# Performance work log

Measured on AMD Instinct MI355X. Metric: run time of the kernel, lower is better.

Reference implementation:

```python
import jax, jax.numpy as jnp
import numpy as np

EPS = 1e-5
B, CIN, L = 512, 5, 1024   # batch, input channels, msp length == d_model
COUT, A, NB = 32, 13, 5    # CNN branch channels, max_atoms, num_bonds_prediction


def conv1d(x, w, pad, groups=1):
    # x: (N, C, L), w: (O, I/groups, K)
    return jax.lax.conv_general_dilated(
        x, w, window_strides=(1,), padding=[(pad, pad)],
        dimension_numbers=("NCH", "OIH", "NCH"), feature_group_count=groups)


def batchnorm(x, g, b):
    # training-mode BN over (N, L) per channel, as nn.BatchNorm1d in train()
    m = jnp.mean(x, axis=(0, 2), keepdims=True)
    v = jnp.var(x, axis=(0, 2), keepdims=True)
    return (x - m) * jax.lax.rsqrt(v + EPS) * g[None, :, None] + b[None, :, None]


def setup_inputs() -> dict:
    key = jax.random.key(0)
    ks = jax.random.split(key, 16)
    n = jax.random.normal
    inp = {
        "src": n(ks[0], (B, CIN, L), dtype=jnp.float32),
        "mask": jnp.ones((B, A), dtype=bool),
        "max_atoms": A,
        # CNN branch 1 (kernel 5) : depthwise, pointwise, BN, residual 1x1 conv
        "dw1": n(ks[1], (CIN, 1, 5), dtype=jnp.float32) * 0.2,
        "pw1": n(ks[2], (COUT, CIN, 1), dtype=jnp.float32) * 0.2,
        "g1": jnp.ones((COUT,), jnp.float32),
        "be1": jnp.zeros((COUT,), jnp.float32),
        "r1w": n(ks[3], (COUT, CIN, 1), dtype=jnp.float32) * 0.2,
        "r1b": jnp.zeros((COUT,), jnp.float32),
        # CNN branch 2 (kernel 3)
        "dw2": n(ks[4], (CIN, 1, 3), dtype=jnp.float32) * 0.2,
        "pw2": n(ks[5], (COUT, CIN, 1), dtype=jnp.float32) * 0.2,
        "g2": jnp.ones((COUT,), jnp.float32),
        "be2": jnp.zeros((COUT,), jnp.float32),
        "r2w": n(ks[6], (COUT, CIN, 1), dtype=jnp.float32) * 0.2,
        "r2b": jnp.zeros((COUT,), jnp.float32),
        # EdgeClassify2 linears: ll1 (2*COUT -> A), fl (2*L -> NB)
        "ll1w": n(ks[7], (A, 2 * COUT), dtype=jnp.float32) * 0.1,
        "ll1b": jnp.zeros((A,), jnp.float32),
        "flw": n(ks[8], (NB, 2 * L), dtype=jnp.float32) * 0.02,
        "flb": jnp.zeros((NB,), jnp.float32),
    }
    return inp


def reference(src, mask, max_atoms, dw1, pw1, g1, be1, r1w, r1b,
              dw2, pw2, g2, be2, r2w, r2b, ll1w, ll1b, flw, flb):
    # ---- CNN encoder ----
    e1 = jax.nn.relu(batchnorm(conv1d(conv1d(src, dw1, 2, groups=CIN), pw1, 0), g1, be1))
    e1 = e1 * (conv1d(src, r1w, 0) + r1b[None, :, None])
    e2 = jax.nn.relu(batchnorm(conv1d(conv1d(src, dw2, 1, groups=CIN), pw2, 0), g2, be2))
    e2 = e2 * (conv1d(src, r2w, 0) + r2b[None, :, None])
    x = jnp.concatenate([e1, e2], axis=1)          # (B, 2*COUT, L)
    # ---- EdgeClassify2 ----
    # ll1 over channel dim: (B, 2*COUT, L) -> (B, A, L)
    h = jnp.einsum("bcl,ac->bal", x, ll1w) + ll1b[None, :, None]
    # vectorized replacement of the O(A^2) python loop:
    # final_e[:, i, j] = concat(h[:, min(i,j)], h[:, max(i,j)])
    idx = jnp.arange(max_atoms)
    mn = jnp.minimum(idx[:, None], idx[None, :])   # (A, A)
    mx = jnp.maximum(idx[:, None], idx[None, :])
    final_e = jnp.concatenate([h[:, mn, :], h[:, mx, :]], axis=-1)  # (B, A, A, 2L)
    out = jnp.einsum("bijd,nd->bijn", final_e, flw) + flb           # (B, A, A, NB)
    return out
```

## Files before the change

kernel.cpp:

```cpp
#include <hip/hip_runtime.h>
#include <hip/hip_bf16.h>

#define BB 512
#define LL 1024
#define AA 13
#define NBP 5
#define NTOT (BB * LL)
#define EPSV 1e-5f

#define WS_F     192
#define WS_PART  256
#define WS_CONST 10496
#define WS_FLW   16384

typedef __attribute__((ext_vector_type(8))) short bhalf8;
typedef __attribute__((ext_vector_type(4))) float floatx4;

__device__ __forceinline__ void trunc_pair(float e0, float e1, unsigned int& hp, unsigned int& lp) {
    unsigned int u0 = __float_as_uint(e0), u1 = __float_as_uint(e1);
    unsigned int h0 = u0 & 0xFFFF0000u, h1 = u1 & 0xFFFF0000u;
    hp = (h0 >> 16) | h1;
    float l0 = e0 - __uint_as_float(h0);
    float l1 = e1 - __uint_as_float(h1);
    lp = (__float_as_uint(l0) >> 16) | (__float_as_uint(l1) & 0xFFFF0000u);
}

template<int CTRL, int RM, bool BC>
__device__ __forceinline__ float dppadd(float v) {
    int t = __builtin_amdgcn_update_dpp(0, __float_as_int(v), CTRL, RM, 0xf, BC);
    return v + __int_as_float(t);
}
__device__ __forceinline__ float wave_sum(float v) {
    v = dppadd<0x111, 0xf, true >(v);
    v = dppadd<0x112, 0xf, true >(v);
    v = dppadd<0x114, 0xf, true >(v);
    v = dppadd<0x118, 0xf, true >(v);
    v = dppadd<0x142, 0xa, false>(v);
    v = dppadd<0x143, 0xc, false>(v);
    return v;
}

__global__ __launch_bounds__(256) void k_moments(
    const float* __restrict__ src,
    const float* __restrict__ dw1,
    const float* __restrict__ dw2,
    const float* __restrict__ flw,
    float* __restrict__ ws)
{
    __shared__ float red[4][40];
    __shared__ float fred[4];
    int tid = threadIdx.x;
    int gid = blockIdx.x * 256 + tid;
    int b = gid >> 7, L0 = (gid & 127) << 3;
    const float* sb = src + b * (5 * LL);

    float w1[5][5], w2[5][3];
#pragma unroll
    for (int c = 0; c < 5; c++) {
#pragma unroll
        for (int t = 0; t < 5; t++) w1[c][t] = dw1[c*5+t];
#pragma unroll
        for (int t = 0; t < 3; t++) w2[c][t] = dw2[c*3+t];
    }

    float x[5][16];
#pragma unroll
    for (int c5 = 0; c5 < 5; c5++) {
        const float* sp = sb + c5 * LL;
        float4 xa = (L0 >= 4)    ? *(const float4*)(sp + L0 - 4) : make_float4(0,0,0,0);
        float4 xb = *(const float4*)(sp + L0);
        float4 xc = *(const float4*)(sp + L0 + 4);
        float4 xd = (L0 <= 1012) ? *(const float4*)(sp + L0 + 8) : make_float4(0,0,0,0);
        x[c5][0]=xa.x; x[c5][1]=xa.y; x[c5][2]=xa.z; x[c5][3]=xa.w;
        x[c5][4]=xb.x; x[c5][5]=xb.y; x[c5][6]=xb.z; x[c5][7]=xb.w;
        x[c5][8]=xc.x; x[c5][9]=xc.y; x[c5][10]=xc.z; x[c5][11]=xc.w;
        x[c5][12]=xd.x; x[c5][13]=xd.y; x[c5][14]=xd.z; x[c5][15]=xd.w;
    }

    float acc[40];
#pragma unroll
    for (int k = 0; k < 40; k++) acc[k] = 0.f;

#pragma unroll
    for (int k = 0; k < 8; k++) {
        float d1[5], d2[5];
#pragma unroll
        for (int c5 = 0; c5 < 5; c5++) {
            d1[c5] = w1[c5][0]*x[c5][k+2] + w1[c5][1]*x[c5][k+3] + w1[c5][2]*x[c5][k+4]
                   + w1[c5][3]*x[c5][k+5] + w1[c5][4]*x[c5][k+6];
            d2[c5] = w2[c5][0]*x[c5][k+3] + w2[c5][1]*x[c5][k+4] + w2[c5][2]*x[c5][k+5];
        }
#pragma unroll
        for (int j = 0; j < 5; j++) { acc[j] += d1[j]; acc[20+j] += d2[j]; }
#pragma unroll
        for (int j = 0; j < 5; j++)
#pragma unroll
            for (int kk = j; kk < 5; kk++) {
                int idx = j*(11-j)/2 + (kk - j);
                acc[5+idx]  += d1[j]*d1[kk];
                acc[25+idx] += d2[j]*d2[kk];
            }
    }

    int lane = tid & 63, wv = tid >> 6;
#pragma unroll
    for (int k = 0; k < 40; k++) acc[k] = wave_sum(acc[k]);
    if (lane == 63) {
#pragma unroll
        for (int k = 0; k < 40; k++) red[wv][k] = acc[k];
    }
    __syncthreads();
    if (tid < 40) {
        ws[WS_PART + blockIdx.x * 40 + tid] =
            red[0][tid] + red[1][tid] + red[2][tid] + red[3][tid];
    }

    if (blockIdx.x < 10) {
        int nn = blockIdx.x;
        int n = nn < 5 ? nn : nn - 5;
        int off = nn < 5 ? 0 : LL;
        float4 v = *(const float4*)(flw + n * (2*LL) + off + tid * 4);
        {
            unsigned int hp0, lp0, hp1, lp1;
            trunc_pair(v.x, v.y, hp0, lp0);
            trunc_pair(v.z, v.w, hp1, lp1);
            char* fwb = (char*)(ws + WS_FLW);
            *(uint2*)(fwb + nn * 2048 + tid * 8)         = make_uint2(hp0, hp1);
            *(uint2*)(fwb + 32768 + nn * 2048 + tid * 8) = make_uint2(lp0, lp1);
        }
        float s = wave_sum(v.x + v.y + v.z + v.w);
        if (lane == 63) fred[wv] = s;
        __syncthreads();
        if (tid == 0) ws[WS_F + nn] = fred[0] + fred[1] + fred[2] + fred[3];
    } else if (blockIdx.x < 16) {
        int nn = blockIdx.x;
        char* fwb = (char*)(ws + WS_FLW);
        *(uint2*)(fwb + nn * 2048 + tid * 8)         = make_uint2(0u, 0u);
        *(uint2*)(fwb + 32768 + nn * 2048 + tid * 8) = make_uint2(0u, 0u);
    }
}

__global__ __launch_bounds__(320) void k_prep(
    float* __restrict__ ws,
    const float* __restrict__ pw1, const float* __restrict__ pw2,
    const float* __restrict__ g1,  const float* __restrict__ be1,
    const float* __restrict__ g2,  const float* __restrict__ be2,
    const float* __restrict__ r1w, const float* __restrict__ r2w,
    const float* __restrict__ r1b, const float* __restrict__ r2b)
{
    __shared__ float momS[40];
    int tid = threadIdx.x;
    {
        int k = tid >> 3, sub = tid & 7;
        float v = 0.f;
#pragma unroll 8
        for (int t2 = 0; t2 < 32; t2++) v += ws[WS_PART + (sub + (t2 << 3)) * 40 + k];
        v += __shfl_xor(v, 1, 64);
        v += __shfl_xor(v, 2, 64);
        v += __shfl_xor(v, 4, 64);
        if (sub == 0) momS[k] = v;
    }
    __syncthreads();
    if (tid < 64) {
        int brc = tid >> 5, o = tid & 31;
        const float invN = 1.0f / (float)NTOT;
        const float* pw = brc ? pw2 : pw1;
        const float* rw = brc ? r2w : r1w;
        const float* s  = momS + (brc ? 20 : 0);
        const float* M  = momS + (brc ? 25 : 5);
        float pwv[5], rwv[5], md[5];
#pragma unroll
        for (int j = 0; j < 5; j++) { pwv[j] = pw[o*5+j]; rwv[j] = rw[o*5+j]; md[j] = s[j] * invN; }
        float meanY = 0.f;
#pragma unroll
        for (int j = 0; j < 5; j++) meanY += pwv[j] * md[j];
        float ey2 = 0.f;
#pragma unroll
        for (int j = 0; j < 5; j++)
#pragma unroll
            for (int k = 0; k < 5; k++) {
                int lo = j < k ? j : k, hi = j < k ? k : j;
                int idx = lo*(11-lo)/2 + (hi - lo);
                ey2 += pwv[j] * pwv[k] * (M[idx] * invN);
            }
        float varY = ey2 - meanY * meanY;
        if (varY < 0.f) varY = 0.f;
        float gg = brc ? g2[o] : g1[o];
        float bb = brc ? be2[o] : be1[o];
        float rb = brc ? r2b[o] : r1b[o];
        float sc = gg * rsqrtf(varY + EPSV);
        float sh = bb - meanY * sc;
        float* dst = ws + WS_CONST + tid * 16;
        dst[0] = pwv[0]*sc; dst[1] = pwv[1]*sc; dst[2] = pwv[2]*sc; dst[3] = pwv[3]*sc;
        dst[4] = pwv[4]*sc; dst[5] = sh;        dst[6] = rb;        dst[7] = 0.f;
        dst[8] = rwv[0];    dst[9] = rwv[1];    dst[10] = rwv[2];   dst[11] = rwv[3];
        dst[12] = rwv[4];   dst[13] = 0.f;      dst[14] = 0.f;      dst[15] = 0.f;
    }
}

__global__ __launch_bounds__(512, 2) void k_fused(
    const float* __restrict__ src,
    const float* __restrict__ dw1,
    const float* __restrict__ dw2,
    const float* __restrict__ ll1w,
    const float* __restrict__ ll1b,
    const float* __restrict__ flb,
    const float* __restrict__ ws_ro,
    float* __restrict__ out)
{
    __shared__ __align__(16) char eBuf[65536];
    __shared__ float llT[832];
    __shared__ float PQ[130];

    int tid = threadIdx.x, b = blockIdx.x;
    int lane = tid & 63;
    int gu = __builtin_amdgcn_readfirstlane(tid >> 6);
    int c0 = gu << 3;
    int br = gu >> 2;
    int mt = gu & 3, kq = gu >> 2;

    const float* srcB = src + b * (5 * LL);

    for (int idx = tid; idx < 832; idx += 512) {
        int cc = idx / 13, a = idx - cc * 13;
        llT[idx] = ll1w[a * 64 + cc];
    }

    float wdw[5][5];
    if (br == 0) {
#pragma unroll
        for (int c5 = 0; c5 < 5; c5++)
#pragma unroll
            for (int t = 0; t < 5; t++) wdw[c5][t] = dw1[c5*5+t];
    } else {
#pragma unroll
        for (int c5 = 0; c5 < 5; c5++) {
            wdw[c5][0] = 0.f;
            wdw[c5][1] = dw2[c5*3+0]; wdw[c5][2] = dw2[c5*3+1]; wdw[c5][3] = dw2[c5*3+2];
            wdw[c5][4] = 0.f;
        }
    }
    const float* cb = ws_ro + WS_CONST + (c0 << 4);

    int nB = lane & 15;
    int kg = (lane >> 4) << 3;
    const char* fwb = (const char*)(ws_ro + WS_FLW);
    floatx4 Cacc = {0.f, 0.f, 0.f, 0.f};

#pragma unroll 1
    for (int p = 0; p < 4; ++p) {
        uint4 bhv[4], blv[4];
#pragma unroll
        for (int k2 = 0; k2 < 4; ++k2) {
            int lg = (p << 8) + (((kq << 2) + k2) << 5) + kg;
            bhv[k2] = *(const uint4*)(fwb + (((nB << 10) + lg) << 1));
            blv[k2] = *(const uint4*)(fwb + 32768 + (((nB << 10) + lg) << 1));
        }

        int l0 = (p << 8) + (lane << 2);
        float dv[5][4], sv[5][4];
#pragma unroll
        for (int c5 = 0; c5 < 5; c5++) {
            const float* s5 = srcB + (c5 << 10);
            float4 xa = (l0 >= 4)    ? *(const float4*)(s5 + l0 - 4) : make_float4(0,0,0,0);
            float4 xb = *(const float4*)(s5 + l0);
            float4 xc = (l0 <= 1016) ? *(const float4*)(s5 + l0 + 4) : make_float4(0,0,0,0);
            float xx[8] = {xa.z, xa.w, xb.x, xb.y, xb.z, xb.w, xc.x, xc.y};
#pragma unroll
            for (int q = 0; q < 4; q++) sv[c5][q] = xx[q + 2];
            if (br == 0) {
#pragma unroll
                for (int q = 0; q < 4; q++)
                    dv[c5][q] = wdw[c5][0]*xx[q] + wdw[c5][1]*xx[q+1] + wdw[c5][2]*xx[q+2]
                              + wdw[c5][3]*xx[q+3] + wdw[c5][4]*xx[q+4];
            } else {
#pragma unroll
                for (int q = 0; q < 4; q++)
                    dv[c5][q] = wdw[c5][1]*xx[q+1] + wdw[c5][2]*xx[q+2] + wdw[c5][3]*xx[q+3];
            }
        }
#pragma unroll
        for (int ci = 0; ci < 8; ci++) {
            const float4 A  = *(const float4*)(cb + ci*16);
            const float4 B2 = *(const float4*)(cb + ci*16 + 4);
            const float4 R0 = *(const float4*)(cb + ci*16 + 8);
            const float4 R1 = *(const float4*)(cb + ci*16 + 12);
            float e[4];
#pragma unroll
            for (int q = 0; q < 4; q++) {
                float y = B2.y + A.x*dv[0][q] + A.y*dv[1][q] + A.z*dv[2][q]
                                + A.w*dv[3][q] + B2.x*dv[4][q];
                float r = B2.z + R0.x*sv[0][q] + R0.y*sv[1][q] + R0.z*sv[2][q]
                                + R0.w*sv[3][q] + R1.x*sv[4][q];
                e[q] = fmaxf(y, 0.f) * r;
            }
            unsigned int hp0, lp0, hp1, lp1;
            trunc_pair(e[0], e[1], hp0, lp0);
            trunc_pair(e[2], e[3], hp1, lp1);
            int c = c0 + ci;
            int off = (c << 10) + ((lane << 3) ^ ((c & 7) << 4));
            *(uint2*)(eBuf + off)       = make_uint2(hp0, hp1);
            *(uint2*)(eBuf + off + 512) = make_uint2(lp0, lp1);
        }
        __syncthreads();

        {
            int ch   = (mt << 4) + (lane & 15);
            int rowb = ch << 10;
            int swz  = (ch & 7) << 4;
#pragma unroll
            for (int k2 = 0; k2 < 4; ++k2) {
                int lbc = (((kq << 2) + k2) << 5) + kg;
                bhalf8 aH = *(const bhalf8*)(eBuf + rowb + ((lbc << 1) ^ swz));
                bhalf8 aL = *(const bhalf8*)(eBuf + rowb + 512 + ((lbc << 1) ^ swz));
                union { uint4 u; bhalf8 v; } bh, bl;
                bh.u = bhv[k2]; bl.u = blv[k2];
                Cacc = __builtin_amdgcn_mfma_f32_16x16x32_bf16(aH, bh.v, Cacc, 0, 0, 0);
                Cacc = __builtin_amdgcn_mfma_f32_16x16x32_bf16(aH, bl.v, Cacc, 0, 0, 0);
                Cacc = __builtin_amdgcn_mfma_f32_16x16x32_bf16(aL, bh.v, Cacc, 0, 0, 0);
            }
        }
        __syncthreads();
    }

    {
        float* part = (float*)eBuf;
        int basep = (gu << 8) + ((lane >> 4) << 6) + (lane & 15);
        part[basep]      = Cacc[0];
        part[basep + 16] = Cacc[1];
        part[basep + 32] = Cacc[2];
        part[basep + 48] = Cacc[3];
    }
    __syncthreads();
    float* SarrF = (float*)eBuf + 4096;
    for (int idx = tid; idx < 1024; idx += 512) {
        int c = idx >> 4, n = idx & 15;
        int mt2 = c >> 4, m = c & 15;
        const float* part = (const float*)eBuf;
        int o = (m << 4) + n;
        SarrF[idx] = part[mt2 * 256 + o] + part[(4 + mt2) * 256 + o];
    }
    __syncthreads();

    if (tid < 130) {
        int half = tid >= 65 ? 1 : 0;
        int q = tid - half * 65;
        int a = q / 5, n = q - a * 5;
        int col = half * 5 + n;
        float v = ll1b[a] * ws_ro[WS_F + col];
#pragma unroll 8
        for (int cc = 0; cc < 64; cc++) v += llT[cc * 13 + a] * SarrF[(cc << 4) + col];
        PQ[tid] = v;
    }
    __syncthreads();

    for (int idx = tid; idx < AA * AA * NBP; idx += 512) {
        int i = idx / 65;
        int rr = idx - i * 65;
        int j = rr / 5, n = rr - j * 5;
        int mn = i < j ? i : j, mx = i < j ? j : i;
        out[b * (AA * AA * NBP) + idx] = PQ[mn * 5 + n] + PQ[65 + mx * 5 + n] + flb[n];
    }
}

extern "C" void kernel_launch(void* const* d_in, const int* in_sizes, int n_in,
                              void* d_out, int out_size, void* d_ws, size_t ws_size,
                              hipStream_t stream) {
    const float* src  = (const float*)d_in[0];
    const float* dw1  = (const float*)d_in[3];
    const float* pw1  = (const float*)d_in[4];
    const float* g1   = (const float*)d_in[5];
    const float* be1  = (const float*)d_in[6];
    const float* r1w  = (const float*)d_in[7];
    const float* r1b  = (const float*)d_in[8];
    const float* dw2  = (const float*)d_in[9];
    const float* pw2  = (const float*)d_in[10];
    const float* g2   = (const float*)d_in[11];
    const float* be2  = (const float*)d_in[12];
    const float* r2w  = (const float*)d_in[13];
    const float* r2b  = (const float*)d_in[14];
    const float* ll1w = (const float*)d_in[15];
    const float* ll1b = (const float*)d_in[16];
    const float* flw  = (const float*)d_in[17];
    const float* flb  = (const float*)d_in[18];
    float* ws  = (float*)d_ws;
    float* out = (float*)d_out;

    k_moments<<<256, 256, 0, stream>>>(src, dw1, dw2, flw, ws);
    k_prep<<<1, 320, 0, stream>>>(ws, pw1, pw2, g1, be1, g2, be2, r1w, r2w, r1b, r2b);
    k_fused<<<BB, 512, 0, stream>>>(src, dw1, dw2, ll1w, ll1b, flb, ws, out);
}
```

Baseline: 147.6 us.

## Halve the LDS activation buffer and precompute depthwise convs in shared memory

The bf16 hi/lo activation tile is now split into two passes through a 32 KB LDS buffer instead of one 64 KB buffer. The low parts are held in registers and written after the high-part MFMAs finish. A new 16x256 float LDS array holds both depthwise-conv branches and the raw source, computed once per chunk by 256 threads instead of redundantly per wave. The goal is lower LDS use, which may allow more resident blocks, plus less redundant global loading and conv arithmetic. The cost is two extra barriers per chunk and more register pressure from the held low parts.

```diff
diff --git a/kernel.cpp b/kernel.cpp
--- a/kernel.cpp
+++ b/kernel.cpp
@@ -208,7 +208,8 @@
     const float* __restrict__ ws_ro,
     float* __restrict__ out)
 {
-    __shared__ __align__(16) char eBuf[65536];
+    __shared__ __align__(16) char eBuf[32768];
+    __shared__ __align__(16) float dvP[16][256];
     __shared__ float llT[832];
     __shared__ float PQ[130];
 
@@ -226,20 +227,6 @@
         llT[idx] = ll1w[a * 64 + cc];
     }
 
-    float wdw[5][5];
-    if (br == 0) {
-#pragma unroll
-        for (int c5 = 0; c5 < 5; c5++)
-#pragma unroll
-            for (int t = 0; t < 5; t++) wdw[c5][t] = dw1[c5*5+t];
-    } else {
-#pragma unroll
-        for (int c5 = 0; c5 < 5; c5++) {
-            wdw[c5][0] = 0.f;
-            wdw[c5][1] = dw2[c5*3+0]; wdw[c5][2] = dw2[c5*3+1]; wdw[c5][3] = dw2[c5*3+2];
-            wdw[c5][4] = 0.f;
-        }
-    }
     const float* cb = ws_ro + WS_CONST + (c0 << 4);
 
     int nB = lane & 15;
@@ -257,28 +244,36 @@
             blv[k2] = *(const uint4*)(fwb + 32768 + (((nB << 10) + lg) << 1));
         }
 
-        int l0 = (p << 8) + (lane << 2);
+        if (tid < 256) {
+            int l = (p << 8) + tid;
+#pragma unroll
+            for (int c5 = 0; c5 < 5; c5++) {
+                const float* s5 = srcB + (c5 << 10);
+                float xm2 = (l >= 2)    ? s5[l - 2] : 0.f;
+                float xm1 = (l >= 1)    ? s5[l - 1] : 0.f;
+                float x0  = s5[l];
+                float xp1 = (l <= 1022) ? s5[l + 1] : 0.f;
+                float xp2 = (l <= 1021) ? s5[l + 2] : 0.f;
+                dvP[c5][tid]      = dw1[c5*5+0]*xm2 + dw1[c5*5+1]*xm1 + dw1[c5*5+2]*x0
+                                  + dw1[c5*5+3]*xp1 + dw1[c5*5+4]*xp2;
+                dvP[5 + c5][tid]  = dw2[c5*3+0]*xm1 + dw2[c5*3+1]*x0 + dw2[c5*3+2]*xp1;
+                dvP[10 + c5][tid] = x0;
+            }
+        }
+        __syncthreads();
+
         float dv[5][4], sv[5][4];
-#pragma unroll
-        for (int c5 = 0; c5 < 5; c5++) {
-            const float* s5 = srcB + (c5 << 10);
-            float4 xa = (l0 >= 4)    ? *(const float4*)(s5 + l0 - 4) : make_float4(0,0,0,0);
-            float4 xb = *(const float4*)(s5 + l0);
-            float4 xc = (l0 <= 1016) ? *(const float4*)(s5 + l0 + 4) : make_float4(0,0,0,0);
-            float xx[8] = {xa.z, xa.w, xb.x, xb.y, xb.z, xb.w, xc.x, xc.y};
-#pragma unroll
-            for (int q = 0; q < 4; q++) sv[c5][q] = xx[q + 2];
-            if (br == 0) {
-#pragma unroll
-                for (int q = 0; q < 4; q++)
-                    dv[c5][q] = wdw[c5][0]*xx[q] + wdw[c5][1]*xx[q+1] + wdw[c5][2]*xx[q+2]
-                              + wdw[c5][3]*xx[q+3] + wdw[c5][4]*xx[q+4];
-            } else {
-#pragma unroll
-                for (int q = 0; q < 4; q++)
-                    dv[c5][q] = wdw[c5][1]*xx[q+1] + wdw[c5][2]*xx[q+2] + wdw[c5][3]*xx[q+3];
-            }
-        }
+        {
+            int lc = lane << 2;
+#pragma unroll
+            for (int c5 = 0; c5 < 5; c5++) {
+                float4 d = *(const float4*)&dvP[br * 5 + c5][lc];
+                float4 s = *(const float4*)&dvP[10 + c5][lc];
+                dv[c5][0]=d.x; dv[c5][1]=d.y; dv[c5][2]=d.z; dv[c5][3]=d.w;
+                sv[c5][0]=s.x; sv[c5][1]=s.y; sv[c5][2]=s.z; sv[c5][3]=s.w;
+            }
+        }
+        uint2 loK[8];
 #pragma unroll
         for (int ci = 0; ci < 8; ci++) {
             const float4 A  = *(const float4*)(cb + ci*16);
@@ -298,31 +293,52 @@
             trunc_pair(e[0], e[1], hp0, lp0);
             trunc_pair(e[2], e[3], hp1, lp1);
             int c = c0 + ci;
-            int off = (c << 10) + ((lane << 3) ^ ((c & 7) << 4));
-            *(uint2*)(eBuf + off)       = make_uint2(hp0, hp1);
-            *(uint2*)(eBuf + off + 512) = make_uint2(lp0, lp1);
+            int off = (c << 9) + ((lane << 3) ^ ((c & 7) << 4));
+            *(uint2*)(eBuf + off) = make_uint2(hp0, hp1);
+            loK[ci] = make_uint2(lp0, lp1);
         }
         __syncthreads();
 
         {
             int ch   = (mt << 4) + (lane & 15);
-            int rowb = ch << 10;
+            int rowb = ch << 9;
             int swz  = (ch & 7) << 4;
 #pragma unroll
             for (int k2 = 0; k2 < 4; ++k2) {
                 int lbc = (((kq << 2) + k2) << 5) + kg;
                 bhalf8 aH = *(const bhalf8*)(eBuf + rowb + ((lbc << 1) ^ swz));
-                bhalf8 aL = *(const bhalf8*)(eBuf + rowb + 512 + ((lbc << 1) ^ swz));
                 union { uint4 u; bhalf8 v; } bh, bl;
                 bh.u = bhv[k2]; bl.u = blv[k2];
                 Cacc = __builtin_amdgcn_mfma_f32_16x16x32_bf16(aH, bh.v, Cacc, 0, 0, 0);
                 Cacc = __builtin_amdgcn_mfma_f32_16x16x32_bf16(aH, bl.v, Cacc, 0, 0, 0);
+            }
+        }
+        __syncthreads();
+
+#pragma unroll
+        for (int ci = 0; ci < 8; ci++) {
+            int c = c0 + ci;
+            int off = (c << 9) + ((lane << 3) ^ ((c & 7) << 4));
+            *(uint2*)(eBuf + off) = loK[ci];
+        }
+        __syncthreads();
+
+        {
+            int ch   = (mt << 4) + (lane & 15);
+            int rowb = ch << 9;
+            int swz  = (ch & 7) << 4;
+#pragma unroll
+            for (int k2 = 0; k2 < 4; ++k2) {
+                int lbc = (((kq << 2) + k2) << 5) + kg;
+                bhalf8 aL = *(const bhalf8*)(eBuf + rowb + ((lbc << 1) ^ swz));
+                union { uint4 u; bhalf8 v; } bh;
+                bh.u = bhv[k2];
                 Cacc = __builtin_amdgcn_mfma_f32_16x16x32_bf16(aL, bh.v, Cacc, 0, 0, 0);
             }
         }
-        __syncthreads();
-    }
-
+    }
+
+    __syncthreads();
     {
         float* part = (float*)eBuf;
         int basep = (gu << 8) + ((lane >> 4) << 6) + (lane & 15);
```

After: 155.1 us. 1.05x slower.
